# Optimization experiments

Hardware: AMD Instinct MI355X
Metric: run time of the kernel (lower is better)

## Reference

```python
import jax, jax.numpy as jnp
import numpy as np

N_EMBD = 768
N_HEAD = 12
B, T = 4, 2048
EPS = 1e-5


def layernorm(x, w, b):
    mu = jnp.mean(x, axis=-1, keepdims=True)
    var = jnp.mean(jnp.square(x - mu), axis=-1, keepdims=True)
    return (x - mu) * jax.lax.rsqrt(var + EPS) * w + b


def setup_inputs() -> dict:
    key = jax.random.key(0)
    ks = jax.random.split(key, 6)
    C = N_EMBD
    s = 0.02
    return {
        "x": jax.random.normal(ks[0], (B, T, C), jnp.float32),
        "ln1_w": jnp.ones((C,), jnp.float32),
        "ln1_b": jnp.zeros((C,), jnp.float32),
        "W_qkv": jax.random.normal(ks[1], (C, 3 * C), jnp.float32) * s,
        "b_qkv": jnp.zeros((3 * C,), jnp.float32),
        "W_attnproj": jax.random.normal(ks[2], (C, C), jnp.float32) * s,
        "b_attnproj": jnp.zeros((C,), jnp.float32),
        "ln2_w": jnp.ones((C,), jnp.float32),
        "ln2_b": jnp.zeros((C,), jnp.float32),
        "W_fc": jax.random.normal(ks[3], (C, 4 * C), jnp.float32) * s,
        "b_fc": jnp.zeros((4 * C,), jnp.float32),
        "W_mlpproj": jax.random.normal(ks[4], (4 * C, C), jnp.float32) * s,
        "b_mlpproj": jnp.zeros((C,), jnp.float32),
    }


def reference(x, ln1_w, ln1_b, W_qkv, b_qkv, W_attnproj, b_attnproj,
              ln2_w, ln2_b, W_fc, b_fc, W_mlpproj, b_mlpproj):
    Bx, Tx, C = x.shape
    H = N_HEAD
    Dh = C // H

    # --- attention branch ---
    h = layernorm(x, ln1_w, ln1_b)
    qkv = h @ W_qkv + b_qkv                       # [B, T, 3C]
    q, k, v = jnp.split(qkv, 3, axis=-1)
    q = q.reshape(Bx, Tx, H, Dh).transpose(0, 2, 1, 3)  # [B, H, T, Dh]
    k = k.reshape(Bx, Tx, H, Dh).transpose(0, 2, 1, 3)
    v = v.reshape(Bx, Tx, H, Dh).transpose(0, 2, 1, 3)
    att = jnp.einsum('bhqd,bhkd->bhqk', q, k) * (1.0 / np.sqrt(Dh))
    att = jax.nn.softmax(att, axis=-1)            # full softmax attention (no mask)
    y = jnp.einsum('bhqk,bhkd->bhqd', att, v)     # [B, H, T, Dh]
    y = y.transpose(0, 2, 1, 3).reshape(Bx, Tx, C)
    y = y @ W_attnproj + b_attnproj
    x = x + y

    # --- MLP branch ---
    h = layernorm(x, ln2_w, ln2_b)
    h = jax.nn.gelu(h @ W_fc + b_fc, approximate=False)
    h = h @ W_mlpproj + b_mlpproj
    return x + h
```

## Files before the change

kernel.cpp:

```cpp
#include <hip/hip_runtime.h>

typedef __bf16 bf16x8 __attribute__((ext_vector_type(8)));
typedef __bf16 bf16x4 __attribute__((ext_vector_type(4)));
typedef float f32x4 __attribute__((ext_vector_type(4)));
typedef unsigned short u16;
typedef unsigned long long u64;

#define GL2LDS(gp, lp) __builtin_amdgcn_global_load_lds(                      \
    (const __attribute__((address_space(1))) void*)(gp),                      \
    (__attribute__((address_space(3))) void*)(lp), 16, 0, 0)

__device__ __forceinline__ u16 f2u(float f) {
    __bf16 h = (__bf16)f;
    return __builtin_bit_cast(u16, h);
}

__device__ __forceinline__ float fexp2(float x) {
    float r;
    asm("v_exp_f32 %0, %1" : "=v"(r) : "v"(x));
    return r;
}

__device__ __forceinline__ float frcp(float x) {
    float r;
    asm("v_rcp_f32 %0, %1" : "=v"(r) : "v"(x));
    return r;
}

__device__ __forceinline__ float gelu(float x) {
    const float a = x * x;
    const float b = fmaf(a, 0.10294323f, 2.30220795f);
    const float u = fexp2(x * b);
    const float r = frcp(1.0f + u);
    return (x > 8.0f) ? x : x * u * r;
}

template <int N>
__device__ __forceinline__ void waitv() {
    if constexpr (N == 0) asm volatile("s_waitcnt vmcnt(0)" ::: "memory");
    else if constexpr (N == 4) asm volatile("s_waitcnt vmcnt(4)" ::: "memory");
    else if constexpr (N == 6) asm volatile("s_waitcnt vmcnt(6)" ::: "memory");
}

__device__ __forceinline__ f32x4 mfma16(bf16x8 a, bf16x8 b, f32x4 c) {
    return __builtin_amdgcn_mfma_f32_16x16x32_bf16(a, b, c, 0, 0, 0);
}

__global__ __launch_bounds__(256) void transpose_kernel(
    const float* __restrict__ W, u16* __restrict__ Wt, int K, int N) {
    __shared__ float tile[32][33];
    const int tx = threadIdx.x & 31, ty = threadIdx.x >> 5;
    const int n0 = blockIdx.x * 32, k0 = blockIdx.y * 32;
#pragma unroll
    for (int i = 0; i < 4; i++)
        tile[ty + 8 * i][tx] = W[(size_t)(k0 + ty + 8 * i) * N + n0 + tx];
    __syncthreads();
#pragma unroll
    for (int i = 0; i < 4; i++)
        Wt[(size_t)(n0 + ty + 8 * i) * K + k0 + tx] = f2u(tile[tx][ty + 8 * i]);
}

__global__ __launch_bounds__(256) void ln_kernel(
    const float* __restrict__ xin, const float* __restrict__ wgt,
    const float* __restrict__ bia, u16* __restrict__ outp) {
    const int row = blockIdx.x, t = threadIdx.x;
    const float* xr = xin + (size_t)row * 768;
    float v0 = xr[t], v1 = xr[t + 256], v2 = xr[t + 512];
    float s = v0 + v1 + v2;
    float ss = v0 * v0 + v1 * v1 + v2 * v2;
#pragma unroll
    for (int off = 32; off; off >>= 1) {
        s += __shfl_xor(s, off);
        ss += __shfl_xor(ss, off);
    }
    __shared__ float red[8];
    const int w = t >> 6;
    if ((t & 63) == 0) { red[w] = s; red[4 + w] = ss; }
    __syncthreads();
    s  = red[0] + red[1] + red[2] + red[3];
    ss = red[4] + red[5] + red[6] + red[7];
    const float mu = s * (1.f / 768.f);
    const float var = ss * (1.f / 768.f) - mu * mu;
    const float rs = rsqrtf(var + 1e-5f);
    u16* orow = outp + (size_t)row * 768;
    orow[t]       = f2u((v0 - mu) * rs * wgt[t]       + bia[t]);
    orow[t + 256] = f2u((v1 - mu) * rs * wgt[t + 256] + bia[t + 256]);
    orow[t + 512] = f2u((v2 - mu) * rs * wgt[t + 512] + bia[t + 512]);
}

template <int EPI>
__global__ __launch_bounds__(256, 3) void gemm_k64(
    const u16* __restrict__ A, const u16* __restrict__ Bt,
    const float* __restrict__ bias, const float* __restrict__ res,
    void* __restrict__ outp, u16* __restrict__ vt, int M, int N, int K) {
    __shared__ __align__(16) u16 As[2][4096];
    __shared__ __align__(16) u16 Bs[2][8192];
    const int t = threadIdx.x;
    const int lane = t & 63, w = t >> 6;
    const int wg0 = blockIdx.y * gridDim.x + blockIdx.x;
    const int xcd = wg0 & 7, loc = wg0 >> 3;
    const int gx = gridDim.x, gy = gridDim.y;
    const int m0 = (xcd * (gy >> 3) + loc / gx) * 64;
    const int n0 = (loc % gx) * 128;
    const int wm = (w >> 1) * 32, wn = (w & 1) * 64;
    const int lq = lane & 15, g = lane >> 4;

    f32x4 acc[2][4];
#pragma unroll
    for (int i = 0; i < 2; i++)
#pragma unroll
        for (int j = 0; j < 4; j++) acc[i][j] = (f32x4){0.f, 0.f, 0.f, 0.f};

    const int srow8 = w * 8 + (lane >> 3);
    const int scol = ((lane & 7) ^ (lane >> 3)) * 8;
    const u16* gA_0 = A + (size_t)(m0 + srow8) * K + scol;
    const u16* gA_1 = A + (size_t)(m0 + 32 + srow8) * K + scol;
    const u16* gB_0 = Bt + (size_t)(n0 + srow8) * K + scol;
    const u16* gB_1 = Bt + (size_t)(n0 + 32 + srow8) * K + scol;
    const u16* gB_2 = Bt + (size_t)(n0 + 64 + srow8) * K + scol;
    const u16* gB_3 = Bt + (size_t)(n0 + 96 + srow8) * K + scol;

    const int KT = K >> 6;

#define STAGE64(buf, kt)                                                      \
    do {                                                                      \
        const int ko_ = (kt) << 6;                                            \
        GL2LDS(gA_0 + ko_, (char*)As[buf] + w * 1024);                        \
        GL2LDS(gA_1 + ko_, (char*)As[buf] + 4096 + w * 1024);                 \
        GL2LDS(gB_0 + ko_, (char*)Bs[buf] + w * 1024);                        \
        GL2LDS(gB_1 + ko_, (char*)Bs[buf] + 4096 + w * 1024);                 \
        GL2LDS(gB_2 + ko_, (char*)Bs[buf] + 8192 + w * 1024);                 \
        GL2LDS(gB_3 + ko_, (char*)Bs[buf] + 12288 + w * 1024);                \
    } while (0)

    STAGE64(0, 0);
    STAGE64(1, 1);
    for (int kt = 0; kt < KT; ++kt) {
        if (kt + 1 < KT) waitv<6>(); else waitv<0>();
        __builtin_amdgcn_s_barrier();
        __builtin_amdgcn_sched_barrier(0);
        const char* aB = (char*)As[kt & 1] + (wm + lq) * 128;
        const char* bB = (char*)Bs[kt & 1] + (wn + lq) * 128;
        const int sw = lq & 7;
#pragma unroll
        for (int s = 0; s < 2; s++) {
            const int co = (((s << 2) + g) ^ sw) << 4;
            bf16x8 af[2], bfr[4];
#pragma unroll
            for (int m = 0; m < 2; m++)
                af[m] = *(const bf16x8*)(aB + m * 2048 + co);
#pragma unroll
            for (int n = 0; n < 4; n++)
                bfr[n] = *(const bf16x8*)(bB + n * 2048 + co);
            __builtin_amdgcn_s_setprio(1);
#pragma unroll
            for (int m = 0; m < 2; m++)
#pragma unroll
                for (int n = 0; n < 4; n++)
                    acc[m][n] = mfma16(af[m], bfr[n], acc[m][n]);
            __builtin_amdgcn_s_setprio(0);
        }
        __builtin_amdgcn_sched_barrier(0);
        __builtin_amdgcn_s_barrier();
        if (kt + 2 < KT) STAGE64(kt & 1, kt + 2);
    }
#undef STAGE64

#pragma unroll
    for (int n = 0; n < 4; n++) {
        const int col = n0 + wn + 16 * n + lq;
        const float bv = bias[col];
#pragma unroll
        for (int m = 0; m < 2; m++) {
            const int rbase = m0 + wm + 16 * m + 4 * g;
            if constexpr (EPI == 0) {
                if (col < 1536) {
                    const float qs = (col < 768) ? 0.18033688f : 1.0f;
#pragma unroll
                    for (int r = 0; r < 4; r++) {
                        const size_t idx = (size_t)(rbase + r) * N + col;
                        ((u16*)outp)[idx] = f2u((acc[m][n][r] + bv) * qs);
                    }
                } else {
                    const int d = col - 1536;
                    bf16x4 pk;
#pragma unroll
                    for (int r = 0; r < 4; r++)
                        pk[r] = (__bf16)(acc[m][n][r] + bv);
                    u16* vrow = vt +
                        ((size_t)((rbase >> 11) * 12 + (d >> 6)) * 64 + (d & 63)) * 2048 +
                        (rbase & 2047);
                    *(u64*)vrow = __builtin_bit_cast(u64, pk);
                }
            } else if constexpr (EPI == 1) {
#pragma unroll
                for (int r = 0; r < 4; r++) {
                    const size_t idx = (size_t)(rbase + r) * N + col;
                    ((float*)outp)[idx] = acc[m][n][r] + bv + res[idx];
                }
            } else {
#pragma unroll
                for (int r = 0; r < 4; r++) {
                    const size_t idx = (size_t)(rbase + r) * N + col;
                    ((u16*)outp)[idx] = f2u(gelu(acc[m][n][r] + bv));
                }
            }
        }
    }
}

__global__ __launch_bounds__(256, 3) void attn_kernel(
    const u16* __restrict__ qkv, const u16* __restrict__ Vt,
    u16* __restrict__ y) {
    __shared__ __align__(16) u16 Ks[2][4096];
    __shared__ __align__(16) u16 Vts[2][4096];
    __shared__ __align__(16) u16 Ps[4][2048];
    const int t = threadIdx.x, lane = t & 63, w = t >> 6;
    int wg = blockIdx.y * gridDim.x + blockIdx.x;
    wg = (wg & 7) * ((gridDim.x * gridDim.y) >> 3) + (wg >> 3);
    const int bh = wg / gridDim.x;
    const int b = bh / 12, h = bh % 12;
    const int q0 = (wg % gridDim.x) * 128 + w * 32;
    const int lq = lane & 15, g = lane >> 4;
    const int swz = (lq & 7) << 4;

    bf16x8 qf[2][2];
#pragma unroll
    for (int qh = 0; qh < 2; qh++) {
        const u16* qp =
            qkv + (size_t)(b * 2048 + q0 + qh * 16 + lq) * 2304 + h * 64 + g * 8;
        qf[qh][0] = *(const bf16x8*)(qp);
        qf[qh][1] = *(const bf16x8*)(qp + 32);
    }
    bf16x8 ones;
#pragma unroll
    for (int i = 0; i < 8; i++) ones[i] = (__bf16)1.0f;

    f32x4 acc_o[2][4], acc_s[2];
#pragma unroll
    for (int qh = 0; qh < 2; qh++) {
        acc_s[qh] = (f32x4){0.f, 0.f, 0.f, 0.f};
#pragma unroll
        for (int f = 0; f < 4; f++) acc_o[qh][f] = (f32x4){0.f, 0.f, 0.f, 0.f};
    }

    const int srow = t >> 3, sc = (t & 7) ^ (srow & 7);
    const u16* kg = qkv + 768 + h * 64 + sc * 8 + (size_t)(b * 2048 + srow) * 2304;
    const u16* vg = Vt + (size_t)(bh * 64 + srow) * 2048 + sc * 8;

#define STAGEKV(buf, kt)                                                      \
    do {                                                                      \
        const int kn_ = (kt) * 64;                                            \
        GL2LDS(kg + (size_t)kn_ * 2304, (char*)Ks[buf] + w * 1024);           \
        GL2LDS(kg + (size_t)(kn_ + 32) * 2304,                                \
               (char*)Ks[buf] + w * 1024 + 4096);                             \
        GL2LDS(vg + kn_, (char*)Vts[buf] + w * 1024);                         \
        GL2LDS(vg + 32 * 2048 + kn_, (char*)Vts[buf] + w * 1024 + 4096);      \
    } while (0)

    STAGEKV(0, 0);
    STAGEKV(1, 1);
    for (int kt = 0; kt < 32; ++kt) {
        const int buf = kt & 1;
        if (kt + 1 < 32) waitv<4>(); else waitv<0>();
        __builtin_amdgcn_s_barrier();
        __builtin_amdgcn_sched_barrier(0);
        const char* KB = (const char*)Ks[buf];
        const char* VB = (const char*)Vts[buf];

        f32x4 st[2][4];
        __builtin_amdgcn_s_setprio(1);
#pragma unroll
        for (int kb = 0; kb < 4; kb++) {
            st[0][kb] = (f32x4){0.f, 0.f, 0.f, 0.f};
            st[1][kb] = (f32x4){0.f, 0.f, 0.f, 0.f};
            const char* kr = KB + (kb * 16 + lq) * 128;
#pragma unroll
            for (int dh = 0; dh < 2; dh++) {
                const bf16x8 kf =
                    *(const bf16x8*)(kr + ((((dh << 2) + g) << 4) ^ swz));
                st[0][kb] = mfma16(kf, qf[0][dh], st[0][kb]);
                st[1][kb] = mfma16(kf, qf[1][dh], st[1][kb]);
            }
        }
        __builtin_amdgcn_s_setprio(0);

#pragma unroll
        for (int qh = 0; qh < 2; qh++) {
            char* pw = (char*)Ps[w] + (qh * 16 + lq) * 128 + ((g & 1) << 3);
#pragma unroll
            for (int kb = 0; kb < 4; kb++) {
                bf16x4 pb;
#pragma unroll
                for (int r = 0; r < 4; r++)
                    pb[r] = (__bf16)fexp2(st[qh][kb][r]);
                *(u64*)(pw + ((((kb << 1) + (g >> 1)) << 4) ^ swz)) =
                    __builtin_bit_cast(u64, pb);
            }
        }

        __builtin_amdgcn_s_setprio(1);
#pragma unroll
        for (int kk = 0; kk < 2; kk++) {
            const int co = ((kk << 2) + g) << 4;
            bf16x8 vf[4];
#pragma unroll
            for (int f = 0; f < 4; f++)
                vf[f] = *(const bf16x8*)(VB + (16 * f + lq) * 128 + (co ^ swz));
#pragma unroll
            for (int qh = 0; qh < 2; qh++) {
                const bf16x8 pf = *(const bf16x8*)(
                    (const char*)Ps[w] + (qh * 16 + lq) * 128 + (co ^ swz));
#pragma unroll
                for (int f = 0; f < 4; f++)
                    acc_o[qh][f] = mfma16(vf[f], pf, acc_o[qh][f]);
                acc_s[qh] = mfma16(ones, pf, acc_s[qh]);
            }
        }
        __builtin_amdgcn_s_setprio(0);
        __builtin_amdgcn_sched_barrier(0);
        __builtin_amdgcn_s_barrier();
        if (kt + 2 < 32) STAGEKV(buf, kt + 2);
    }
#undef STAGEKV

#pragma unroll
    for (int qh = 0; qh < 2; qh++) {
        const float rinv = frcp(acc_s[qh][0]);
        char* yb = (char*)(y + (size_t)(b * 2048 + q0 + qh * 16 + lq) * 768 +
                           h * 64);
#pragma unroll
        for (int f = 0; f < 4; f++) {
            bf16x4 pk;
#pragma unroll
            for (int r = 0; r < 4; r++) pk[r] = (__bf16)(acc_o[qh][f][r] * rinv);
            *(u64*)(yb + f * 32 + g * 8) = __builtin_bit_cast(u64, pk);
        }
    }
}

extern "C" void kernel_launch(void* const* d_in, const int* in_sizes, int n_in,
                              void* d_out, int out_size, void* d_ws,
                              size_t ws_size, hipStream_t stream) {
    const float* x    = (const float*)d_in[0];
    const float* ln1w = (const float*)d_in[1];
    const float* ln1b = (const float*)d_in[2];
    const float* Wqkv = (const float*)d_in[3];
    const float* bqkv = (const float*)d_in[4];
    const float* Wap  = (const float*)d_in[5];
    const float* bap  = (const float*)d_in[6];
    const float* ln2w = (const float*)d_in[7];
    const float* ln2b = (const float*)d_in[8];
    const float* Wfc  = (const float*)d_in[9];
    const float* bfc  = (const float*)d_in[10];
    const float* Wmp  = (const float*)d_in[11];
    const float* bmp  = (const float*)d_in[12];
    float* out = (float*)d_out;

    char* ws = (char*)d_ws;
    u16* Wt_qkv = (u16*)(ws);
    u16* Wt_ap  = (u16*)(ws + 3538944);
    u16* Wt_fc  = (u16*)(ws + 4718592);
    u16* Wt_mp  = (u16*)(ws + 9437184);
    u16* bufA   = (u16*)(ws + 14155776);
    u16* bufB   = (u16*)(ws + 26738688);
    u16* VtBuf  = (u16*)(ws + 64487424);

    transpose_kernel<<<dim3(72, 24), 256, 0, stream>>>(Wqkv, Wt_qkv, 768, 2304);
    transpose_kernel<<<dim3(24, 24), 256, 0, stream>>>(Wap, Wt_ap, 768, 768);
    transpose_kernel<<<dim3(96, 24), 256, 0, stream>>>(Wfc, Wt_fc, 768, 3072);
    transpose_kernel<<<dim3(24, 96), 256, 0, stream>>>(Wmp, Wt_mp, 3072, 768);

    ln_kernel<<<8192, 256, 0, stream>>>(x, ln1w, ln1b, bufA);
    gemm_k64<0><<<dim3(18, 128), 256, 0, stream>>>(
        bufA, Wt_qkv, bqkv, nullptr, bufB, VtBuf, 8192, 2304, 768);
    attn_kernel<<<dim3(16, 48), 256, 0, stream>>>(bufB, VtBuf, bufA);
    gemm_k64<1><<<dim3(6, 128), 256, 0, stream>>>(
        bufA, Wt_ap, bap, x, out, nullptr, 8192, 768, 768);
    ln_kernel<<<8192, 256, 0, stream>>>(out, ln2w, ln2b, bufA);
    gemm_k64<2><<<dim3(24, 128), 256, 0, stream>>>(
        bufA, Wt_fc, bfc, nullptr, bufB, nullptr, 8192, 3072, 768);
    gemm_k64<1><<<dim3(6, 128), 256, 0, stream>>>(
        bufB, Wt_mp, bmp, out, out, nullptr, 8192, 768, 3072);
}
```

Measured before the change: 265.5 us.

## Switch GEMMs to 128x128 tiles with K=32 stages and shrink attention P buffer

The GEMM kernel moves from 64x128 output tiles with a K step of 64 to 128x128 tiles with a K step of 32. LDS shrinks, so the occupancy hint rises to 4 and each wave computes a 4x4 MFMA block, giving more reuse per loaded fragment. The attention kernel halves its per-wave P scratch by writing and consuming P in two K-halves interleaved with the PV MFMAs, with a new swizzle. The price is more accumulator registers per wave, twice as many barriers per K, and fewer blocks for the N=768 GEMMs (384 blocks).

```diff
diff --git a/kernel.cpp b/kernel.cpp
--- a/kernel.cpp
+++ b/kernel.cpp
@@ -39,7 +39,6 @@
 __device__ __forceinline__ void waitv() {
     if constexpr (N == 0) asm volatile("s_waitcnt vmcnt(0)" ::: "memory");
     else if constexpr (N == 4) asm volatile("s_waitcnt vmcnt(4)" ::: "memory");
-    else if constexpr (N == 6) asm volatile("s_waitcnt vmcnt(6)" ::: "memory");
 }
 
 __device__ __forceinline__ f32x4 mfma16(bf16x8 a, bf16x8 b, f32x4 c) {
@@ -89,89 +88,79 @@
 }
 
 template <int EPI>
-__global__ __launch_bounds__(256, 3) void gemm_k64(
+__global__ __launch_bounds__(256, 4) void gemm32(
     const u16* __restrict__ A, const u16* __restrict__ Bt,
     const float* __restrict__ bias, const float* __restrict__ res,
     void* __restrict__ outp, u16* __restrict__ vt, int M, int N, int K) {
     __shared__ __align__(16) u16 As[2][4096];
-    __shared__ __align__(16) u16 Bs[2][8192];
+    __shared__ __align__(16) u16 Bs[2][4096];
     const int t = threadIdx.x;
     const int lane = t & 63, w = t >> 6;
     const int wg0 = blockIdx.y * gridDim.x + blockIdx.x;
     const int xcd = wg0 & 7, loc = wg0 >> 3;
     const int gx = gridDim.x, gy = gridDim.y;
-    const int m0 = (xcd * (gy >> 3) + loc / gx) * 64;
+    const int m0 = (xcd * (gy >> 3) + loc / gx) * 128;
     const int n0 = (loc % gx) * 128;
-    const int wm = (w >> 1) * 32, wn = (w & 1) * 64;
+    const int wm = (w >> 1) * 64, wn = (w & 1) * 64;
     const int lq = lane & 15, g = lane >> 4;
 
-    f32x4 acc[2][4];
-#pragma unroll
-    for (int i = 0; i < 2; i++)
+    f32x4 acc[4][4];
+#pragma unroll
+    for (int i = 0; i < 4; i++)
 #pragma unroll
         for (int j = 0; j < 4; j++) acc[i][j] = (f32x4){0.f, 0.f, 0.f, 0.f};
 
-    const int srow8 = w * 8 + (lane >> 3);
-    const int scol = ((lane & 7) ^ (lane >> 3)) * 8;
-    const u16* gA_0 = A + (size_t)(m0 + srow8) * K + scol;
-    const u16* gA_1 = A + (size_t)(m0 + 32 + srow8) * K + scol;
-    const u16* gB_0 = Bt + (size_t)(n0 + srow8) * K + scol;
-    const u16* gB_1 = Bt + (size_t)(n0 + 32 + srow8) * K + scol;
-    const u16* gB_2 = Bt + (size_t)(n0 + 64 + srow8) * K + scol;
-    const u16* gB_3 = Bt + (size_t)(n0 + 96 + srow8) * K + scol;
-
-    const int KT = K >> 6;
-
-#define STAGE64(buf, kt)                                                      \
+    const int srow = t >> 2;
+    const int scol = ((t & 3) ^ ((t >> 3) & 3)) * 8;
+    const u16* gA0 = A + (size_t)(m0 + srow) * K + scol;
+    const u16* gA1 = A + (size_t)(m0 + 64 + srow) * K + scol;
+    const u16* gB0 = Bt + (size_t)(n0 + srow) * K + scol;
+    const u16* gB1 = Bt + (size_t)(n0 + 64 + srow) * K + scol;
+
+    const int cph = (g ^ ((lq >> 1) & 3)) << 4;
+    const int KT = K >> 5;
+
+#define STAGE32(buf, kt)                                                      \
     do {                                                                      \
-        const int ko_ = (kt) << 6;                                            \
-        GL2LDS(gA_0 + ko_, (char*)As[buf] + w * 1024);                        \
-        GL2LDS(gA_1 + ko_, (char*)As[buf] + 4096 + w * 1024);                 \
-        GL2LDS(gB_0 + ko_, (char*)Bs[buf] + w * 1024);                        \
-        GL2LDS(gB_1 + ko_, (char*)Bs[buf] + 4096 + w * 1024);                 \
-        GL2LDS(gB_2 + ko_, (char*)Bs[buf] + 8192 + w * 1024);                 \
-        GL2LDS(gB_3 + ko_, (char*)Bs[buf] + 12288 + w * 1024);                \
+        const int ko_ = (kt) << 5;                                            \
+        GL2LDS(gA0 + ko_, (char*)As[buf] + w * 1024);                         \
+        GL2LDS(gA1 + ko_, (char*)As[buf] + 4096 + w * 1024);                  \
+        GL2LDS(gB0 + ko_, (char*)Bs[buf] + w * 1024);                         \
+        GL2LDS(gB1 + ko_, (char*)Bs[buf] + 4096 + w * 1024);                  \
     } while (0)
 
-    STAGE64(0, 0);
-    STAGE64(1, 1);
+    STAGE32(0, 0);
+    STAGE32(1, 1);
     for (int kt = 0; kt < KT; ++kt) {
-        if (kt + 1 < KT) waitv<6>(); else waitv<0>();
+        if (kt + 1 < KT) waitv<4>(); else waitv<0>();
         __builtin_amdgcn_s_barrier();
         __builtin_amdgcn_sched_barrier(0);
-        const char* aB = (char*)As[kt & 1] + (wm + lq) * 128;
-        const char* bB = (char*)Bs[kt & 1] + (wn + lq) * 128;
-        const int sw = lq & 7;
-#pragma unroll
-        for (int s = 0; s < 2; s++) {
-            const int co = (((s << 2) + g) ^ sw) << 4;
-            bf16x8 af[2], bfr[4];
-#pragma unroll
-            for (int m = 0; m < 2; m++)
-                af[m] = *(const bf16x8*)(aB + m * 2048 + co);
+        const char* rA = (char*)As[kt & 1] + (wm + lq) * 64 + cph;
+        const char* rB = (char*)Bs[kt & 1] + (wn + lq) * 64 + cph;
+        bf16x8 af[4], bfr[4];
+#pragma unroll
+        for (int m = 0; m < 4; m++) af[m] = *(const bf16x8*)(rA + m * 1024);
+#pragma unroll
+        for (int n = 0; n < 4; n++) bfr[n] = *(const bf16x8*)(rB + n * 1024);
+        __builtin_amdgcn_s_setprio(1);
+#pragma unroll
+        for (int m = 0; m < 4; m++)
 #pragma unroll
             for (int n = 0; n < 4; n++)
-                bfr[n] = *(const bf16x8*)(bB + n * 2048 + co);
-            __builtin_amdgcn_s_setprio(1);
-#pragma unroll
-            for (int m = 0; m < 2; m++)
-#pragma unroll
-                for (int n = 0; n < 4; n++)
-                    acc[m][n] = mfma16(af[m], bfr[n], acc[m][n]);
-            __builtin_amdgcn_s_setprio(0);
-        }
+                acc[m][n] = mfma16(af[m], bfr[n], acc[m][n]);
+        __builtin_amdgcn_s_setprio(0);
         __builtin_amdgcn_sched_barrier(0);
         __builtin_amdgcn_s_barrier();
-        if (kt + 2 < KT) STAGE64(kt & 1, kt + 2);
-    }
-#undef STAGE64
+        if (kt + 2 < KT) STAGE32(kt & 1, kt + 2);
+    }
+#undef STAGE32
 
 #pragma unroll
     for (int n = 0; n < 4; n++) {
         const int col = n0 + wn + 16 * n + lq;
         const float bv = bias[col];
 #pragma unroll
-        for (int m = 0; m < 2; m++) {
+        for (int m = 0; m < 4; m++) {
             const int rbase = m0 + wm + 16 * m + 4 * g;
             if constexpr (EPI == 0) {
                 if (col < 1536) {
@@ -209,12 +198,12 @@
     }
 }
 
-__global__ __launch_bounds__(256, 3) void attn_kernel(
+__global__ __launch_bounds__(256, 4) void attn_kernel(
     const u16* __restrict__ qkv, const u16* __restrict__ Vt,
     u16* __restrict__ y) {
     __shared__ __align__(16) u16 Ks[2][4096];
     __shared__ __align__(16) u16 Vts[2][4096];
-    __shared__ __align__(16) u16 Ps[4][2048];
+    __shared__ __align__(16) u16 Ps[4][1024];
     const int t = threadIdx.x, lane = t & 63, w = t >> 6;
     int wg = blockIdx.y * gridDim.x + blockIdx.x;
     wg = (wg & 7) * ((gridDim.x * gridDim.y) >> 3) + (wg >> 3);
@@ -286,38 +275,40 @@
         __builtin_amdgcn_s_setprio(0);
 
 #pragma unroll
-        for (int qh = 0; qh < 2; qh++) {
-            char* pw = (char*)Ps[w] + (qh * 16 + lq) * 128 + ((g & 1) << 3);
-#pragma unroll
-            for (int kb = 0; kb < 4; kb++) {
-                bf16x4 pb;
-#pragma unroll
-                for (int r = 0; r < 4; r++)
-                    pb[r] = (__bf16)fexp2(st[qh][kb][r]);
-                *(u64*)(pw + ((((kb << 1) + (g >> 1)) << 4) ^ swz)) =
-                    __builtin_bit_cast(u64, pb);
+        for (int kk = 0; kk < 2; kk++) {
+#pragma unroll
+            for (int qh = 0; qh < 2; qh++) {
+                char* pw = (char*)Ps[w] + (qh * 16 + lq) * 64 + ((g & 1) << 3);
+#pragma unroll
+                for (int kb2 = 0; kb2 < 2; kb2++) {
+                    const int kb = kk * 2 + kb2;
+                    bf16x4 pb;
+#pragma unroll
+                    for (int r = 0; r < 4; r++)
+                        pb[r] = (__bf16)fexp2(st[qh][kb][r]);
+                    *(u64*)(pw +
+                            ((((kb2 << 1) + (g >> 1)) ^ (lq & 3)) << 4)) =
+                        __builtin_bit_cast(u64, pb);
+                }
             }
-        }
-
-        __builtin_amdgcn_s_setprio(1);
-#pragma unroll
-        for (int kk = 0; kk < 2; kk++) {
             const int co = ((kk << 2) + g) << 4;
             bf16x8 vf[4];
 #pragma unroll
             for (int f = 0; f < 4; f++)
                 vf[f] = *(const bf16x8*)(VB + (16 * f + lq) * 128 + (co ^ swz));
+            __builtin_amdgcn_s_setprio(1);
 #pragma unroll
             for (int qh = 0; qh < 2; qh++) {
                 const bf16x8 pf = *(const bf16x8*)(
-                    (const char*)Ps[w] + (qh * 16 + lq) * 128 + (co ^ swz));
+                    (const char*)Ps[w] + (qh * 16 + lq) * 64 +
+                    ((g ^ (lq & 3)) << 4));
 #pragma unroll
                 for (int f = 0; f < 4; f++)
                     acc_o[qh][f] = mfma16(vf[f], pf, acc_o[qh][f]);
                 acc_s[qh] = mfma16(ones, pf, acc_s[qh]);
             }
+            __builtin_amdgcn_s_setprio(0);
         }
-        __builtin_amdgcn_s_setprio(0);
         __builtin_amdgcn_sched_barrier(0);
         __builtin_amdgcn_s_barrier();
         if (kt + 2 < 32) STAGEKV(buf, kt + 2);
@@ -372,14 +363,14 @@
     transpose_kernel<<<dim3(24, 96), 256, 0, stream>>>(Wmp, Wt_mp, 3072, 768);
 
     ln_kernel<<<8192, 256, 0, stream>>>(x, ln1w, ln1b, bufA);
-    gemm_k64<0><<<dim3(18, 128), 256, 0, stream>>>(
+    gemm32<0><<<dim3(18, 64), 256, 0, stream>>>(
         bufA, Wt_qkv, bqkv, nullptr, bufB, VtBuf, 8192, 2304, 768);
     attn_kernel<<<dim3(16, 48), 256, 0, stream>>>(bufB, VtBuf, bufA);
-    gemm_k64<1><<<dim3(6, 128), 256, 0, stream>>>(
+    gemm32<1><<<dim3(6, 64), 256, 0, stream>>>(
         bufA, Wt_ap, bap, x, out, nullptr, 8192, 768, 768);
     ln_kernel<<<8192, 256, 0, stream>>>(out, ln2w, ln2b, bufA);
-    gemm_k64<2><<<dim3(24, 128), 256, 0, stream>>>(
+    gemm32<2><<<dim3(24, 64), 256, 0, stream>>>(
         bufA, Wt_fc, bfc, nullptr, bufB, nullptr, 8192, 3072, 768);
-    gemm_k64<1><<<dim3(6, 128), 256, 0, stream>>>(
+    gemm32<1><<<dim3(6, 64), 256, 0, stream>>>(
         bufB, Wt_mp, bmp, out, out, nullptr, 8192, 768, 3072);
 }
```

After: 302.2 us. 13.8% more time.
